# Performance work log

Measured on AMD Instinct MI355X. Metric: run time of the kernel, lower is better.

Reference implementation:

```python
import jax, jax.numpy as jnp
import numpy as np

N, E, B = 131072, 262144, 4096
NODE_DIM, EDGE_DIM, HIDDEN = 16, 4, 64
MLP_HID = 128


def setup_inputs() -> dict:
    key = jax.random.key(0)
    ks = jax.random.split(key, 16)
    def nrm(k, shape, s=0.05):
        return jax.random.normal(k, shape, jnp.float32) * s
    return {
        "x": jax.random.normal(ks[0], (N, NODE_DIM), jnp.float32),
        "edge_attr": jax.random.normal(ks[1], (E, EDGE_DIM), jnp.float32),
        "edge_index": jax.random.randint(ks[2], (2, E), 0, N),
        "batch": jnp.sort(jax.random.randint(ks[3], (N,), 0, B)),
        "w_e1": nrm(ks[4], (EDGE_DIM, MLP_HID)),
        "b_e1": jnp.zeros((MLP_HID,), jnp.float32),
        "w_e2": nrm(ks[5], (MLP_HID, NODE_DIM * HIDDEN)),
        "b_e2": jnp.zeros((NODE_DIM * HIDDEN,), jnp.float32),
        "root": nrm(ks[6], (NODE_DIM, HIDDEN)),
        "conv_bias": jnp.zeros((HIDDEN,), jnp.float32),
        "gru_wih": nrm(ks[7], (3 * HIDDEN, HIDDEN)),
        "gru_whh": nrm(ks[8], (3 * HIDDEN, HIDDEN)),
        "gru_bih": jnp.zeros((3 * HIDDEN,), jnp.float32),
        "gru_bhh": jnp.zeros((3 * HIDDEN,), jnp.float32),
        "lstm_wih": nrm(ks[9], (4 * HIDDEN, 2 * HIDDEN)),
        "lstm_whh": nrm(ks[10], (4 * HIDDEN, HIDDEN)),
        "lstm_bih": jnp.zeros((4 * HIDDEN,), jnp.float32),
        "lstm_bhh": jnp.zeros((4 * HIDDEN,), jnp.float32),
        "fc1_w": nrm(ks[11], (2 * HIDDEN, HIDDEN)),
        "fc1_b": jnp.zeros((HIDDEN,), jnp.float32),
        "fc2_w": nrm(ks[12], (HIDDEN, 1)),
        "fc2_b": jnp.zeros((1,), jnp.float32),
    }


def reference(x, edge_attr, edge_index, batch,
              w_e1, b_e1, w_e2, b_e2, root, conv_bias,
              gru_wih, gru_whh, gru_bih, gru_bhh,
              lstm_wih, lstm_whh, lstm_bih, lstm_bhh,
              fc1_w, fc1_b, fc2_w, fc2_b):
    src, dst = edge_index[0], edge_index[1]
    # NNConv: edge-MLP -> per-edge weight [E, node_dim, hidden]
    Wdyn = (jax.nn.relu(edge_attr @ w_e1 + b_e1) @ w_e2 + b_e2).reshape(E, NODE_DIM, HIDDEN)
    msg = jnp.einsum('ed,edh->eh', x[src], Wdyn)  # gather + per-edge matmul
    msum = jax.ops.segment_sum(msg, dst, num_segments=N)
    cnt = jax.ops.segment_sum(jnp.ones((E,), msg.dtype), dst, num_segments=N)
    agg = msum / jnp.maximum(cnt, 1.0)[:, None]  # scatter-mean
    out = jax.nn.relu(agg + x @ root + conv_bias)
    h = out
    for _ in range(3):
        gi = out @ gru_wih.T + gru_bih
        gh = h @ gru_whh.T + gru_bhh
        ir, iz, inn = jnp.split(gi, 3, axis=-1)
        hr, hz, hn = jnp.split(gh, 3, axis=-1)
        r = jax.nn.sigmoid(ir + hr)
        z = jax.nn.sigmoid(iz + hz)
        n = jnp.tanh(inn + r * hn)
        h = (1.0 - z) * n + z * h
        out = h
    # Set2Set, 3 processing steps
    hl = jnp.zeros((B, HIDDEN), out.dtype)
    cl = jnp.zeros((B, HIDDEN), out.dtype)
    q_star = jnp.zeros((B, 2 * HIDDEN), out.dtype)
    for _ in range(3):
        gates = q_star @ lstm_wih.T + lstm_bih + hl @ lstm_whh.T + lstm_bhh
        ig, fg, gg, og = jnp.split(gates, 4, axis=-1)
        ig = jax.nn.sigmoid(ig); fg = jax.nn.sigmoid(fg)
        gg = jnp.tanh(gg); og = jax.nn.sigmoid(og)
        cl = fg * cl + ig * gg
        hl = og * jnp.tanh(cl)
        q = hl  # [B, H]
        e = jnp.sum(out * q[batch], axis=-1)  # [N]
        m = jax.lax.stop_gradient(jax.ops.segment_max(e, batch, num_segments=B))
        ex = jnp.exp(e - m[batch])
        denom = jax.ops.segment_sum(ex, batch, num_segments=B)
        a = ex / denom[batch]  # segment softmax
        r_g = jax.ops.segment_sum(a[:, None] * out, batch, num_segments=B)
        q_star = jnp.concatenate([q, r_g], axis=-1)
    y = jax.nn.relu(q_star @ fc1_w + fc1_b)
    return (y @ fc2_w + fc2_b).squeeze(-1)
```

## Files before the change

### kernel.cpp

```cpp
#include <hip/hip_runtime.h>
#include <math.h>

#define N_NODES 131072
#define N_EDGES 262144
#define N_B     4096

typedef __attribute__((ext_vector_type(8))) short short8;
typedef __attribute__((ext_vector_type(8))) _Float16 half8;
typedef __attribute__((ext_vector_type(4))) float f32x4;
typedef __attribute__((ext_vector_type(16))) float f32x16;

__device__ __forceinline__ float fast_sig(float x) {
    return 1.0f / (1.0f + __expf(-x));
}
__device__ __forceinline__ float fast_tanh(float x) {
    float t = __expf(-2.0f * fabsf(x));
    float r = (1.0f - t) / (1.0f + t);
    return copysignf(r, x);
}

__device__ __forceinline__ void load_lds16(const void* g, void* l) {
    __builtin_amdgcn_global_load_lds(
        (const __attribute__((address_space(1))) unsigned int*)g,
        (__attribute__((address_space(3))) unsigned int*)l, 16, 0, 0);
}

__global__ __launch_bounds__(256) void k_misc(
    const float* __restrict__ we2, unsigned short* __restrict__ wt,
    const float* __restrict__ gwih, const float* __restrict__ gwhh,
    const float* __restrict__ gbih, const float* __restrict__ gbhh,
    unsigned short* __restrict__ wtg, float* __restrict__ gbias,
    const float* __restrict__ lwih, const float* __restrict__ lwhh,
    float4* __restrict__ wA, float4* __restrict__ wB,
    const int* __restrict__ batch, int* __restrict__ starts,
    const int* __restrict__ eidx, int* __restrict__ deg)
{
    const int bid = blockIdx.x;
    const int tid = threadIdx.x;
    if (bid >= 105) {
        int p = (bid - 105) * 256 + tid;
        atomicAdd(&deg[eidx[N_EDGES + p]], 1);
        return;
    }
    if (bid < 64) {
        int p = bid * 256 + tid;
        int d = p >> 10;
        int u = (p >> 9) & 1;
        int s = (p >> 6) & 7;
        int l = p & 63;
        int k0 = s * 16 + ((l >> 5) << 3);
        int h = u * 32 + (l & 31);
        half8 hv;
        #pragma unroll
        for (int j = 0; j < 8; ++j) {
            float v = we2[(size_t)(k0 + j) * 1024 + d * 64 + h];
            hv[j] = (_Float16)v;
        }
        size_t base = (size_t)d * 8192 + (size_t)u * 4096 + s * 512 + l * 8;
        *(half8*)&wt[base] = hv;
    } else if (bid < 72) {
        int p = (bid - 64) * 256 + tid;
        if (p < 256) {
            int g = p >> 6, j = p & 63;
            float b;
            if (g == 0)      b = gbih[j] + gbhh[j];
            else if (g == 1) b = gbih[64 + j] + gbhh[64 + j];
            else if (g == 2) b = gbih[128 + j];
            else             b = gbhh[128 + j];
            gbias[p] = b;
        }
        int u = p >> 7, ks = (p >> 6) & 1, ln = p & 63;
        int n = u * 16 + (ln & 15);
        int g = n >> 6, jn = n & 63;
        int k0 = ks * 32 + (ln >> 4) * 8;
        half8 hv;
        #pragma unroll
        for (int jj = 0; jj < 8; ++jj) {
            int k = k0 + jj;
            float v;
            if (g == 0)      v = gwih[jn * 64 + k] + gwhh[jn * 64 + k];
            else if (g == 1) v = gwih[(64 + jn) * 64 + k] + gwhh[(64 + jn) * 64 + k];
            else if (g == 2) v = gwih[(128 + jn) * 64 + k];
            else             v = gwhh[(128 + jn) * 64 + k];
            hv[jj] = (_Float16)v;
        }
        size_t base = (size_t)(u * 2 + ks) * 512 + ln * 8;
        *(half8*)&wtg[base] = hv;
    } else if (bid < 88) {
        int p = (bid - 72) * 256 + tid;
        int k = p >> 6, ln = p & 63;
        float4 a, b;
        a.x = lwih[(0 * 64 + ln) * 128 + k] + lwhh[(0 * 64 + ln) * 64 + k];
        a.y = lwih[(1 * 64 + ln) * 128 + k] + lwhh[(1 * 64 + ln) * 64 + k];
        a.z = lwih[(2 * 64 + ln) * 128 + k] + lwhh[(2 * 64 + ln) * 64 + k];
        a.w = lwih[(3 * 64 + ln) * 128 + k] + lwhh[(3 * 64 + ln) * 64 + k];
        b.x = lwih[(0 * 64 + ln) * 128 + 64 + k];
        b.y = lwih[(1 * 64 + ln) * 128 + 64 + k];
        b.z = lwih[(2 * 64 + ln) * 128 + 64 + k];
        b.w = lwih[(3 * 64 + ln) * 128 + 64 + k];
        wA[p] = a; wB[p] = b;
    } else {
        int g = (bid - 88) * 256 + tid;
        if (g > N_B) return;
        if (g == N_B) { starts[N_B] = N_NODES; return; }
        int lo = 0, hi = N_NODES;
        while (lo < hi) {
            int mid = (lo + hi) >> 1;
            if (batch[mid] < g) lo = mid + 1; else hi = mid;
        }
        starts[g] = lo;
    }
}

__global__ __launch_bounds__(256) void k_scan1(
    const int* __restrict__ deg, int* __restrict__ psum)
{
    __shared__ int sm[256];
    const int t = threadIdx.x;
    sm[t] = deg[blockIdx.x * 256 + t];
    __syncthreads();
    #pragma unroll
    for (int off = 128; off; off >>= 1) {
        if (t < off) sm[t] += sm[t + off];
        __syncthreads();
    }
    if (t == 0) psum[blockIdx.x] = sm[0];
}

__global__ __launch_bounds__(512) void k_scan2(
    const int* __restrict__ psum, int* __restrict__ psumx)
{
    __shared__ int sm[512];
    const int t = threadIdx.x;
    sm[t] = psum[t];
    __syncthreads();
    #pragma unroll
    for (int off = 1; off < 512; off <<= 1) {
        int add = (t >= off) ? sm[t - off] : 0;
        __syncthreads();
        sm[t] += add;
        __syncthreads();
    }
    psumx[t] = (t > 0) ? sm[t - 1] : 0;
}

__global__ __launch_bounds__(256) void k_scan3(
    const int* __restrict__ deg, const int* __restrict__ psumx,
    int* __restrict__ row_ptr, int* __restrict__ cursor)
{
    __shared__ int sm[256];
    const int t = threadIdx.x;
    const int i = blockIdx.x * 256 + t;
    int d = deg[i];
    sm[t] = d;
    __syncthreads();
    #pragma unroll
    for (int off = 1; off < 256; off <<= 1) {
        int add = (t >= off) ? sm[t - off] : 0;
        __syncthreads();
        sm[t] += add;
        __syncthreads();
    }
    int excl = sm[t] - d + psumx[blockIdx.x];
    row_ptr[i] = excl;
    cursor[i] = excl;
    if (i == 0) row_ptr[N_NODES] = N_EDGES;
}

__global__ __launch_bounds__(256) void k_scat(
    const int* __restrict__ eidx, int* __restrict__ cursor,
    int* __restrict__ epos)
{
    int e = blockIdx.x * 256 + threadIdx.x;
    int dst = eidx[N_EDGES + e];
    epos[e] = atomicAdd(&cursor[dst], 1);
}

__global__ __launch_bounds__(512)
__attribute__((amdgpu_waves_per_eu(4, 8)))
void k_edge(
    const float* __restrict__ x,
    const float* __restrict__ ea,
    const int*   __restrict__ eidx,
    const int*   __restrict__ epos,
    const float* __restrict__ we1,
    const float* __restrict__ be1,
    const unsigned short* __restrict__ wt,
    const float* __restrict__ be2,
    float* __restrict__ emsg)
{
    __shared__ __attribute__((aligned(16))) char smem[62464];
    unsigned short* sAh  = (unsigned short*)smem;
    float* sxT  = (float*)(smem + 49152);
    float* sbe2 = (float*)(smem + 57856);
    int*   spos = (int*)(smem + 61952);

    const int tid = threadIdx.x;
    const int w   = tid >> 6;
    const int ln  = tid & 63;
    const int u   = w >> 2;
    const int mt  = w & 3;
    const int eb  = blockIdx.x * 128;
    const int d0  = blockIdx.x & 15;

    #pragma unroll
    for (int r = 0; r < 2; ++r) {
        int seg = r * 8 + w;
        load_lds16(wt + (size_t)d0 * 8192 + seg * 512 + ln * 8,
                   smem + 32768 + seg * 1024);
    }

    if (tid < 128) spos[tid] = epos[eb + tid];
    #pragma unroll
    for (int v = tid; v < 1024; v += 512) sbe2[v] = be2[v];

    {
        int e = tid >> 2, q = tid & 3;
        int src = eidx[eb + e];
        float4 t4 = ((const float4*)(x + (size_t)src * 16))[q];
        sxT[(q * 4 + 0) * 136 + e] = t4.x;
        sxT[(q * 4 + 1) * 136 + e] = t4.y;
        sxT[(q * 4 + 2) * 136 + e] = t4.z;
        sxT[(q * 4 + 3) * 136 + e] = t4.w;
    }

    #pragma unroll 1
    for (int i = 0; i < 4; ++i) {
        int cc = tid + i * 512;
        int mtc = cc >> 9;
        int s  = (cc >> 6) & 7;
        int l  = cc & 63;
        int e   = mtc * 32 + (l & 31);
        int kk0 = s * 16 + ((l >> 5) << 3);
        float4 eav = *(const float4*)(ea + (size_t)(eb + e) * 4);
        float4 b0 = *(const float4*)(be1 + kk0);
        float4 b1 = *(const float4*)(be1 + kk0 + 4);
        float acc[8] = {b0.x, b0.y, b0.z, b0.w, b1.x, b1.y, b1.z, b1.w};
        #pragma unroll
        for (int a = 0; a < 4; ++a) {
            float4 wa0 = *(const float4*)(we1 + a * 128 + kk0);
            float4 wa1 = *(const float4*)(we1 + a * 128 + kk0 + 4);
            float ev = (a == 0) ? eav.x : (a == 1) ? eav.y : (a == 2) ? eav.z : eav.w;
            acc[0] += ev * wa0.x; acc[1] += ev * wa0.y;
            acc[2] += ev * wa0.z; acc[3] += ev * wa0.w;
            acc[4] += ev * wa1.x; acc[5] += ev * wa1.y;
            acc[6] += ev * wa1.z; acc[7] += ev * wa1.w;
        }
        half8 hv;
        #pragma unroll
        for (int j = 0; j < 8; ++j) {
            hv[j] = (_Float16)fmaxf(acc[j], 0.0f);
        }
        *(half8*)&sAh[cc * 8] = hv;
    }
    __syncthreads();

    half8 ah[8];
    #pragma unroll
    for (int s = 0; s < 8; ++s) {
        ah[s] = *(half8*)&sAh[((mt * 8 + s) * 64 + ln) * 8];
    }
    #pragma unroll
    for (int s = 0; s < 8; ++s) {
        asm volatile("" : "+v"(ah[s]));
    }
    __syncthreads();

    {
        int dn = (d0 + 1) & 15;
        #pragma unroll
        for (int r = 0; r < 2; ++r) {
            int seg = r * 8 + w;
            load_lds16(wt + (size_t)dn * 8192 + seg * 512 + ln * 8,
                       smem + 0 + seg * 1024);
        }
    }

    const int rbase = (ln >> 5) * 4;

    f32x16 msg;
    #pragma unroll
    for (int r = 0; r < 16; ++r) msg[r] = 0.0f;

    int m = 0;
    #pragma unroll 1
    for (int dd = 0; dd < 16; ++dd) {
        const int d = (d0 + dd) & 15;

        if (dd == 15) asm volatile("s_waitcnt vmcnt(0)" ::: "memory");
        else          asm volatile("s_waitcnt vmcnt(2)" ::: "memory");
        __builtin_amdgcn_s_barrier();
        __builtin_amdgcn_sched_barrier(0);

        const unsigned short* bcur =
            (const unsigned short*)(smem + (m == 0 ? 32768 : (m == 1 ? 0 : 16384)));

        float bv = sbe2[d * 64 + u * 32 + (ln & 31)];
        f32x16 c2;
        #pragma unroll
        for (int r = 0; r < 16; ++r) c2[r] = bv;

        #pragma unroll
        for (int s = 0; s < 8; ++s) {
            half8 bb = *(const half8*)&bcur[u * 4096 + s * 512 + ln * 8];
            c2 = __builtin_amdgcn_mfma_f32_32x32x16_f16(ah[s], bb, c2, 0, 0, 0);
        }
        #pragma unroll
        for (int q = 0; q < 4; ++q) {
            f32x4 xv = *(const f32x4*)&sxT[d * 136 + mt * 32 + rbase + 8 * q];
            #pragma unroll
            for (int j = 0; j < 4; ++j) {
                msg[q * 4 + j] = fmaf(xv[j], c2[q * 4 + j], msg[q * 4 + j]);
            }
        }

        if (dd + 2 < 16) {
            int dn = (d0 + dd + 2) & 15;
            int mn = (m == 0) ? 2 : (m == 1 ? 0 : 1);
            char* db = smem + (mn == 0 ? 32768 : (mn == 1 ? 0 : 16384));
            #pragma unroll
            for (int r = 0; r < 2; ++r) {
                int seg = r * 8 + w;
                load_lds16(wt + (size_t)dn * 8192 + seg * 512 + ln * 8,
                           db + seg * 1024);
            }
        }
        m = (m == 2) ? 0 : m + 1;
    }

    const int col = u * 32 + (ln & 31);
    #pragma unroll
    for (int r = 0; r < 16; ++r) {
        int row = (r & 3) + ((r >> 2) * 8) + rbase;
        int pos = spos[mt * 32 + row];
        emsg[(size_t)pos * 64 + col] = msg[r];
    }
}

__global__ __launch_bounds__(256, 2) void k_gru2(
    float* __restrict__ buf,
    const float* __restrict__ emsg,
    const int* __restrict__ rowp,
    const float* __restrict__ x,
    const float* __restrict__ root,
    const float* __restrict__ cb,
    const unsigned short* __restrict__ wtg,
    const float* __restrict__ gbias)
{
    __shared__ unsigned short sAh[8192];
    __shared__ float sroot[1024];
    __shared__ float sbias[256];
    __shared__ float scb[64];
    const int tid = threadIdx.x;
    const int w = tid >> 6, ln = tid & 63, lq = ln >> 4, lm = ln & 15;
    const size_t nbase = (size_t)blockIdx.x * 128;

    #pragma unroll
    for (int v = tid; v < 1024; v += 256) sroot[v] = root[v];
    sbias[tid] = gbias[tid];
    if (tid < 64) scb[tid] = cb[tid];
    __syncthreads();

    #pragma unroll 2
    for (int i = 0; i < 4; ++i) {
        int cc = tid + i * 256;
        int mt = cc >> 7, ks = (cc >> 6) & 1, l = cc & 63;
        size_t gn = nbase + mt * 16 + (l & 15);
        int c0 = ks * 32 + (l >> 4) * 8;
        int rp0 = rowp[gn], rp1 = rowp[gn + 1];
        float ms[8] = {0.f, 0.f, 0.f, 0.f, 0.f, 0.f, 0.f, 0.f};
        for (int k = rp0; k < rp1; ++k) {
            float4 m0 = *(const float4*)(emsg + (size_t)k * 64 + c0);
            float4 m1 = *(const float4*)(emsg + (size_t)k * 64 + c0 + 4);
            ms[0] += m0.x; ms[1] += m0.y; ms[2] += m0.z; ms[3] += m0.w;
            ms[4] += m1.x; ms[5] += m1.y; ms[6] += m1.z; ms[7] += m1.w;
        }
        float cinv = 1.0f / fmaxf((float)(rp1 - rp0), 1.0f);
        float xv[16];
        *(float4*)&xv[0]  = *(const float4*)(x + gn * 16);
        *(float4*)&xv[4]  = *(const float4*)(x + gn * 16 + 4);
        *(float4*)&xv[8]  = *(const float4*)(x + gn * 16 + 8);
        *(float4*)&xv[12] = *(const float4*)(x + gn * 16 + 12);
        float acc[8];
        #pragma unroll
        for (int j = 0; j < 8; ++j) acc[j] = scb[c0 + j];
        #pragma unroll
        for (int d = 0; d < 16; ++d) {
            float xd = xv[d];
            #pragma unroll
            for (int j = 0; j < 8; ++j) acc[j] += xd * sroot[d * 64 + c0 + j];
        }
        half8 hv;
        #pragma unroll
        for (int j = 0; j < 8; ++j) {
            float hval = fmaxf(ms[j] * cinv + acc[j], 0.0f);
            hv[j] = (_Float16)hval;
        }
        *(half8*)&sAh[cc * 8] = hv;
    }
    __syncthreads();

    #pragma unroll 1
    for (int step = 0; step < 3; ++step) {
        half8 ah[2][2];
        #pragma unroll
        for (int i = 0; i < 2; ++i)
            #pragma unroll
            for (int ks = 0; ks < 2; ++ks) {
                int mt = w * 2 + i;
                ah[i][ks] = *(half8*)&sAh[((mt * 2 + ks) * 64 + ln) * 8];
            }
        __syncthreads();

        #pragma unroll 1
        for (int v = 0; v < 4; ++v) {
            f32x4 C[4][2];
            #pragma unroll
            for (int g = 0; g < 4; ++g) {
                float bv = sbias[g * 64 + v * 16 + lm];
                #pragma unroll
                for (int i = 0; i < 2; ++i) C[g][i] = (f32x4){bv, bv, bv, bv};
            }
            #pragma unroll
            for (int g = 0; g < 4; ++g) {
                int u = g * 4 + v;
                #pragma unroll
                for (int ks = 0; ks < 2; ++ks) {
                    size_t wb = (size_t)(u * 2 + ks) * 512 + ln * 8;
                    half8 bb = *(const half8*)&wtg[wb];
                    #pragma unroll
                    for (int i = 0; i < 2; ++i) {
                        C[g][i] = __builtin_amdgcn_mfma_f32_16x16x32_f16(ah[i][ks], bb, C[g][i], 0, 0, 0);
                    }
                }
            }
            int ksp = v >> 1;
            int lq2 = (v & 1) * 2 + (lm >> 3);
            int jp = lm & 7;
            #pragma unroll
            for (int i = 0; i < 2; ++i) {
                int mt = w * 2 + i;
                #pragma unroll
                for (int r = 0; r < 4; ++r) {
                    int idx = ((mt * 2 + ksp) * 64 + lq2 * 16 + lq * 4 + r) * 8 + jp;
                    float hold = (float)*(const _Float16*)&sAh[idx];
                    float rr = fast_sig(C[0][i][r]);
                    float zz = fast_sig(C[1][i][r]);
                    float nn = fast_tanh(C[2][i][r] + rr * C[3][i][r]);
                    float hnew = (1.0f - zz) * nn + zz * hold;
                    if (step < 2) {
                        _Float16 hh = (_Float16)hnew;
                        sAh[idx] = *(unsigned short*)&hh;
                    } else {
                        buf[(nbase + mt * 16 + lq * 4 + r) * 64 + v * 16 + lm] = hnew;
                    }
                }
            }
        }
        if (step < 2) __syncthreads();
    }
}

__global__ __launch_bounds__(256) void k_s2s(
    const float* __restrict__ out,
    const int*   __restrict__ starts,
    const float4* __restrict__ wA,
    const float4* __restrict__ wB,
    const float* __restrict__ bih,
    const float* __restrict__ bhh,
    const float* __restrict__ fc1w,
    const float* __restrict__ fc1b,
    const float* __restrict__ fc2w,
    const float* __restrict__ fc2b,
    float* __restrict__ y)
{
    __shared__ float osh[4][32][66];
    __shared__ float qsL[4][128];
    __shared__ float ebuf[4][256];
    const int tid = threadIdx.x;
    const int wv = tid >> 6, ln = tid & 63;
    const int gid = blockIdx.x * 4 + wv;

    const int s0 = starts[gid];
    int L = starts[gid + 1] - s0; if (L > 256) L = 256;
    const int SL = (L < 32) ? L : 32;

    #pragma unroll
    for (int base = 0; base < 32; base += 4) {
        int row = base + (ln >> 4);
        int c4 = (ln & 15) * 4;
        if (row < SL)
            *(float4*)&osh[wv][row][c4] =
                *(const float4*)(out + (size_t)(s0 + row) * 64 + c4);
    }

    qsL[wv][ln] = 0.0f; qsL[wv][64 + ln] = 0.0f;
    __builtin_amdgcn_wave_barrier();

    const float b0 = bih[ln] + bhh[ln];
    const float b1 = bih[64 + ln] + bhh[64 + ln];
    const float b2 = bih[128 + ln] + bhh[128 + ln];
    const float b3 = bih[192 + ln] + bhh[192 + ln];

    float c = 0.0f;

    #pragma unroll 1
    for (int step = 0; step < 3; ++step) {
        float a0 = b0, a1 = b1, a2 = b2, a3 = b3;
        #pragma unroll 4
        for (int k = 0; k < 64; ++k) {
            float qk = qsL[wv][k];
            float rk = qsL[wv][64 + k];
            float4 wa = wA[k * 64 + ln];
            float4 wb = wB[k * 64 + ln];
            a0 += wa.x * qk + wb.x * rk;
            a1 += wa.y * qk + wb.y * rk;
            a2 += wa.z * qk + wb.z * rk;
            a3 += wa.w * qk + wb.w * rk;
        }
        float ig = fast_sig(a0), fg = fast_sig(a1);
        float gg = fast_tanh(a2), og = fast_sig(a3);
        c = fg * c + ig * gg;
        float h = og * fast_tanh(c);
        __builtin_amdgcn_wave_barrier();
        qsL[wv][ln] = h;
        __builtin_amdgcn_wave_barrier();

        float m = -1e30f;
        for (int c0 = 0; c0 * 64 < L; ++c0) {
            int j = c0 * 64 + ln;
            if (j < L) {
                float a = 0.0f;
                if (j < SL) {
                    #pragma unroll
                    for (int l4 = 0; l4 < 16; ++l4) {
                        float4 ov = *(const float4*)&osh[wv][j][l4 * 4];
                        float4 hv = *(const float4*)&qsL[wv][l4 * 4];
                        a += ov.x * hv.x + ov.y * hv.y + ov.z * hv.z + ov.w * hv.w;
                    }
                } else {
                    const float4* orow = (const float4*)(out + (size_t)(s0 + j) * 64);
                    #pragma unroll
                    for (int l4 = 0; l4 < 16; ++l4) {
                        float4 ov = orow[l4];
                        float4 hv = *(const float4*)&qsL[wv][l4 * 4];
                        a += ov.x * hv.x + ov.y * hv.y + ov.z * hv.z + ov.w * hv.w;
                    }
                }
                ebuf[wv][j] = a;
                m = fmaxf(m, a);
            }
        }
        #pragma unroll
        for (int off = 32; off; off >>= 1) m = fmaxf(m, __shfl_xor(m, off));
        float ds = 0.0f;
        for (int c0 = 0; c0 * 64 < L; ++c0) {
            int j = c0 * 64 + ln;
            if (j < L) {
                float ex = __expf(ebuf[wv][j] - m);
                ebuf[wv][j] = ex;
                ds += ex;
            }
        }
        #pragma unroll
        for (int off = 32; off; off >>= 1) ds += __shfl_xor(ds, off);
        __builtin_amdgcn_wave_barrier();
        float rg = 0.0f;
        for (int j = 0; j < SL; ++j)
            rg = fmaf(ebuf[wv][j], osh[wv][j][ln], rg);
        for (int j = SL; j < L; ++j)
            rg = fmaf(ebuf[wv][j], out[(size_t)(s0 + j) * 64 + ln], rg);
        rg = (L > 0) ? (rg / ds) : 0.0f;
        qsL[wv][64 + ln] = rg;
        __builtin_amdgcn_wave_barrier();
    }

    float a = fc1b[ln];
    #pragma unroll 4
    for (int k = 0; k < 128; ++k)
        a = fmaf(qsL[wv][k], fc1w[k * 64 + ln], a);
    float uu = fmaxf(a, 0.0f) * fc2w[ln];
    #pragma unroll
    for (int off = 32; off; off >>= 1) uu += __shfl_xor(uu, off);
    if (ln == 0) y[gid] = uu + fc2b[0];
}

extern "C" void kernel_launch(void* const* d_in, const int* in_sizes, int n_in,
                              void* d_out, int out_size, void* d_ws, size_t ws_size,
                              hipStream_t stream) {
    const float* x     = (const float*)d_in[0];
    const float* ea    = (const float*)d_in[1];
    const int*   eidx  = (const int*)d_in[2];
    const int*   batch = (const int*)d_in[3];
    const float* we1   = (const float*)d_in[4];
    const float* be1   = (const float*)d_in[5];
    const float* we2   = (const float*)d_in[6];
    const float* be2   = (const float*)d_in[7];
    const float* root  = (const float*)d_in[8];
    const float* cb    = (const float*)d_in[9];
    const float* gwih  = (const float*)d_in[10];
    const float* gwhh  = (const float*)d_in[11];
    const float* gbih  = (const float*)d_in[12];
    const float* gbhh  = (const float*)d_in[13];
    const float* lwih  = (const float*)d_in[14];
    const float* lwhh  = (const float*)d_in[15];
    const float* lbih  = (const float*)d_in[16];
    const float* lbhh  = (const float*)d_in[17];
    const float* fc1w  = (const float*)d_in[18];
    const float* fc1b  = (const float*)d_in[19];
    const float* fc2w  = (const float*)d_in[20];
    const float* fc2b  = (const float*)d_in[21];

    float* emsg = (float*)d_ws;
    float* buf  = emsg + (size_t)N_EDGES * 64;
    int* deg    = (int*)(buf + (size_t)N_NODES * 64);
    int* cursor = deg + N_NODES;
    int* rowp   = cursor + N_NODES;
    int* epos   = rowp + N_NODES + 1;
    int* psum   = epos + N_EDGES;
    int* psumx  = psum + 512;
    int* starts = psumx + 512;
    size_t off = (size_t)((char*)(starts + N_B + 1) - (char*)d_ws);
    off = (off + 15) & ~(size_t)15;
    unsigned short* wt  = (unsigned short*)((char*)d_ws + off);
    unsigned short* wtg = wt + 262144;
    float* gbias = (float*)(wtg + 32768);
    float4* wA = (float4*)(gbias + 256);
    float4* wB = wA + 4096;
    float* y = (float*)d_out;

    hipMemsetAsync(deg, 0, (size_t)N_NODES * sizeof(int), stream);
    k_misc<<<1129, 256, 0, stream>>>(we2, wt, gwih, gwhh, gbih, gbhh, wtg, gbias,
                                     lwih, lwhh, wA, wB, batch, starts, eidx, deg);
    k_scan1<<<512, 256, 0, stream>>>(deg, psum);
    k_scan2<<<1, 512, 0, stream>>>(psum, psumx);
    k_scan3<<<512, 256, 0, stream>>>(deg, psumx, rowp, cursor);
    k_scat<<<1024, 256, 0, stream>>>(eidx, cursor, epos);
    k_edge<<<N_EDGES / 128, 512, 0, stream>>>(x, ea, eidx, epos, we1, be1, wt, be2, emsg);
    k_gru2<<<N_NODES / 128, 256, 0, stream>>>(buf, emsg, rowp, x, root, cb,
                                              wtg, gbias);
    k_s2s<<<N_B / 4, 256, 0, stream>>>(buf, starts, wA, wB, lbih, lbhh,
                                       fc1w, fc1b, fc2w, fc2b, y);
}
```

Baseline: 354.3 us.

## Double edges per block in k_edge so each B tile feeds two MFMAs

Each k_edge block now handles 256 edges instead of 128. Every wave keeps two A fragments and two accumulators, so each half8 of the dynamic weight tile read from LDS feeds two MFMAs. This halves how often the per-d weight slab must be streamed from global into LDS per edge. In exchange LDS grows to about 104KB per block and registers per thread roughly double, which cuts occupancy to about two blocks per CU and halves the grid size.

```diff
diff --git a/kernel.cpp b/kernel.cpp
--- a/kernel.cpp
+++ b/kernel.cpp
@@ -176,8 +176,7 @@
     epos[e] = atomicAdd(&cursor[dst], 1);
 }
 
-__global__ __launch_bounds__(512)
-__attribute__((amdgpu_waves_per_eu(4, 8)))
+__global__ __launch_bounds__(512, 2)
 void k_edge(
     const float* __restrict__ x,
     const float* __restrict__ ea,
@@ -189,43 +188,44 @@
     const float* __restrict__ be2,
     float* __restrict__ emsg)
 {
-    __shared__ __attribute__((aligned(16))) char smem[62464];
+    __shared__ __attribute__((aligned(16))) char smem[103936];
     unsigned short* sAh  = (unsigned short*)smem;
-    float* sxT  = (float*)(smem + 49152);
-    float* sbe2 = (float*)(smem + 57856);
-    int*   spos = (int*)(smem + 61952);
+    float* sxT  = (float*)(smem + 65536);
+    float* sbe2 = (float*)(smem + 82432);
+    int*   spos = (int*)(smem + 86528);
 
     const int tid = threadIdx.x;
     const int w   = tid >> 6;
     const int ln  = tid & 63;
     const int u   = w >> 2;
-    const int mt  = w & 3;
-    const int eb  = blockIdx.x * 128;
+    const int mp  = w & 3;
+    const int eb  = blockIdx.x * 256;
     const int d0  = blockIdx.x & 15;
 
     #pragma unroll
     for (int r = 0; r < 2; ++r) {
         int seg = r * 8 + w;
         load_lds16(wt + (size_t)d0 * 8192 + seg * 512 + ln * 8,
-                   smem + 32768 + seg * 1024);
-    }
-
-    if (tid < 128) spos[tid] = epos[eb + tid];
+                   smem + 87552 + seg * 1024);
+    }
+
+    if (tid < 256) spos[tid] = epos[eb + tid];
     #pragma unroll
     for (int v = tid; v < 1024; v += 512) sbe2[v] = be2[v];
 
-    {
-        int e = tid >> 2, q = tid & 3;
+    #pragma unroll
+    for (int v = tid; v < 1024; v += 512) {
+        int e = v >> 2, q = v & 3;
         int src = eidx[eb + e];
         float4 t4 = ((const float4*)(x + (size_t)src * 16))[q];
-        sxT[(q * 4 + 0) * 136 + e] = t4.x;
-        sxT[(q * 4 + 1) * 136 + e] = t4.y;
-        sxT[(q * 4 + 2) * 136 + e] = t4.z;
-        sxT[(q * 4 + 3) * 136 + e] = t4.w;
+        sxT[(q * 4 + 0) * 264 + e] = t4.x;
+        sxT[(q * 4 + 1) * 264 + e] = t4.y;
+        sxT[(q * 4 + 2) * 264 + e] = t4.z;
+        sxT[(q * 4 + 3) * 264 + e] = t4.w;
     }
 
     #pragma unroll 1
-    for (int i = 0; i < 4; ++i) {
+    for (int i = 0; i < 8; ++i) {
         int cc = tid + i * 512;
         int mtc = cc >> 9;
         int s  = (cc >> 6) & 7;
@@ -255,14 +255,15 @@
     }
     __syncthreads();
 
-    half8 ah[8];
+    half8 ah0[8], ah1[8];
     #pragma unroll
     for (int s = 0; s < 8; ++s) {
-        ah[s] = *(half8*)&sAh[((mt * 8 + s) * 64 + ln) * 8];
+        ah0[s] = *(half8*)&sAh[(((mp * 2 + 0) * 8 + s) * 64 + ln) * 8];
+        ah1[s] = *(half8*)&sAh[(((mp * 2 + 1) * 8 + s) * 64 + ln) * 8];
     }
     #pragma unroll
     for (int s = 0; s < 8; ++s) {
-        asm volatile("" : "+v"(ah[s]));
+        asm volatile("" : "+v"(ah0[s]), "+v"(ah1[s]));
     }
     __syncthreads();
 
@@ -278,9 +279,9 @@
 
     const int rbase = (ln >> 5) * 4;
 
-    f32x16 msg;
-    #pragma unroll
-    for (int r = 0; r < 16; ++r) msg[r] = 0.0f;
+    f32x16 msg0, msg1;
+    #pragma unroll
+    for (int r = 0; r < 16; ++r) { msg0[r] = 0.0f; msg1[r] = 0.0f; }
 
     int m = 0;
     #pragma unroll 1
@@ -293,31 +294,34 @@
         __builtin_amdgcn_sched_barrier(0);
 
         const unsigned short* bcur =
-            (const unsigned short*)(smem + (m == 0 ? 32768 : (m == 1 ? 0 : 16384)));
+            (const unsigned short*)(smem + (m == 0 ? 87552 : (m == 1 ? 0 : 16384)));
 
         float bv = sbe2[d * 64 + u * 32 + (ln & 31)];
-        f32x16 c2;
-        #pragma unroll
-        for (int r = 0; r < 16; ++r) c2[r] = bv;
+        f32x16 c20, c21;
+        #pragma unroll
+        for (int r = 0; r < 16; ++r) { c20[r] = bv; c21[r] = bv; }
 
         #pragma unroll
         for (int s = 0; s < 8; ++s) {
             half8 bb = *(const half8*)&bcur[u * 4096 + s * 512 + ln * 8];
-            c2 = __builtin_amdgcn_mfma_f32_32x32x16_f16(ah[s], bb, c2, 0, 0, 0);
+            c20 = __builtin_amdgcn_mfma_f32_32x32x16_f16(ah0[s], bb, c20, 0, 0, 0);
+            c21 = __builtin_amdgcn_mfma_f32_32x32x16_f16(ah1[s], bb, c21, 0, 0, 0);
         }
         #pragma unroll
         for (int q = 0; q < 4; ++q) {
-            f32x4 xv = *(const f32x4*)&sxT[d * 136 + mt * 32 + rbase + 8 * q];
+            f32x4 xv0 = *(const f32x4*)&sxT[d * 264 + (mp * 2 + 0) * 32 + rbase + 8 * q];
+            f32x4 xv1 = *(const f32x4*)&sxT[d * 264 + (mp * 2 + 1) * 32 + rbase + 8 * q];
             #pragma unroll
             for (int j = 0; j < 4; ++j) {
-                msg[q * 4 + j] = fmaf(xv[j], c2[q * 4 + j], msg[q * 4 + j]);
+                msg0[q * 4 + j] = fmaf(xv0[j], c20[q * 4 + j], msg0[q * 4 + j]);
+                msg1[q * 4 + j] = fmaf(xv1[j], c21[q * 4 + j], msg1[q * 4 + j]);
             }
         }
 
         if (dd + 2 < 16) {
             int dn = (d0 + dd + 2) & 15;
             int mn = (m == 0) ? 2 : (m == 1 ? 0 : 1);
-            char* db = smem + (mn == 0 ? 32768 : (mn == 1 ? 0 : 16384));
+            char* db = smem + (mn == 0 ? 87552 : (mn == 1 ? 0 : 16384));
             #pragma unroll
             for (int r = 0; r < 2; ++r) {
                 int seg = r * 8 + w;
@@ -332,8 +336,10 @@
     #pragma unroll
     for (int r = 0; r < 16; ++r) {
         int row = (r & 3) + ((r >> 2) * 8) + rbase;
-        int pos = spos[mt * 32 + row];
-        emsg[(size_t)pos * 64 + col] = msg[r];
+        int pos0 = spos[(mp * 2 + 0) * 32 + row];
+        int pos1 = spos[(mp * 2 + 1) * 32 + row];
+        emsg[(size_t)pos0 * 64 + col] = msg0[r];
+        emsg[(size_t)pos1 * 64 + col] = msg1[r];
     }
 }
 
@@ -636,7 +642,7 @@
     k_scan2<<<1, 512, 0, stream>>>(psum, psumx);
     k_scan3<<<512, 256, 0, stream>>>(deg, psumx, rowp, cursor);
     k_scat<<<1024, 256, 0, stream>>>(eidx, cursor, epos);
-    k_edge<<<N_EDGES / 128, 512, 0, stream>>>(x, ea, eidx, epos, we1, be1, wt, be2, emsg);
+    k_edge<<<N_EDGES / 256, 512, 0, stream>>>(x, ea, eidx, epos, we1, be1, wt, be2, emsg);
     k_gru2<<<N_NODES / 128, 256, 0, stream>>>(buf, emsg, rowp, x, root, cb,
                                               wtg, gbias);
     k_s2s<<<N_B / 4, 256, 0, stream>>>(buf, starts, wA, wB, lbih, lbhh,
```

Measured after the change: 357.8 us. About the same (+1.0%).
